# Performance work log

Measured on AMD Instinct MI355X. Metric: run time of the kernel, lower is better.

Reference implementation:

```python
import jax, jax.numpy as jnp
import numpy as np

H = 1024   # hidden_dim
D = 256    # dynamics_dim
L = 2      # gru layers
BS = 1024  # batch
T = 256    # max_len
# activation layout over D: softmax[0:32], softmax[32:47], sigmoid[47:48], sigmoid[48:256]
CAT1 = 32
CAT2_SM_END = 47

def setup_inputs():
    key = jax.random.key(0)
    ks = jax.random.split(key, 12)
    s = 0.02
    return {
        "embed": jax.random.normal(ks[0], (BS, H * (1 + L)), jnp.float32),
        "dynamics": jax.random.uniform(ks[1], (BS, T, D), jnp.float32),
        "seq_len": T,
        "W_ih0": s * jax.random.normal(ks[2], (3 * H, H + D), jnp.float32),
        "W_hh0": s * jax.random.normal(ks[3], (3 * H, H), jnp.float32),
        "b_ih0": s * jax.random.normal(ks[4], (3 * H,), jnp.float32),
        "b_hh0": s * jax.random.normal(ks[5], (3 * H,), jnp.float32),
        "W_ih1": s * jax.random.normal(ks[6], (3 * H, H), jnp.float32),
        "W_hh1": s * jax.random.normal(ks[7], (3 * H, H), jnp.float32),
        "b_ih1": s * jax.random.normal(ks[8], (3 * H,), jnp.float32),
        "b_hh1": s * jax.random.normal(ks[9], (3 * H,), jnp.float32),
        "W_fc": s * jax.random.normal(ks[10], (D, H), jnp.float32),
        "b_fc": s * jax.random.normal(ks[11], (D,), jnp.float32),
    }

def gru_cell(inp, h, W_ih, W_hh, b_ih, b_hh):
    # PyTorch GRU cell math
    gi = inp @ W_ih.T + b_ih          # (bs, 3H)
    gh = h @ W_hh.T + b_hh            # (bs, 3H)
    r = jax.nn.sigmoid(gi[:, :H] + gh[:, :H])
    z = jax.nn.sigmoid(gi[:, H:2 * H] + gh[:, H:2 * H])
    n = jnp.tanh(gi[:, 2 * H:] + r * gh[:, 2 * H:])
    return (1.0 - z) * n + z * h

def apply_activation(x):
    # mirrors processors layout: cat(32), cat-missing(15 softmax + 1 sigmoid), cont(208 sigmoid)
    return jnp.concatenate([
        jax.nn.softmax(x[:, :CAT1], axis=-1),
        jax.nn.softmax(x[:, CAT1:CAT2_SM_END], axis=-1),
        jax.nn.sigmoid(x[:, CAT2_SM_END:]),
    ], axis=-1)

def reference(embed, dynamics, seq_len, W_ih0, W_hh0, b_ih0, b_hh0,
              W_ih1, W_hh1, b_ih1, b_hh1, W_fc, b_fc):
    glob = embed[:, :H]                      # (bs, H)
    h0 = embed[:, H:2 * H]                   # layer-0 initial hidden
    h1 = embed[:, 2 * H:3 * H]               # layer-1 initial hidden
    x0 = dynamics[:, 0, :]                   # (bs, D)

    def step(carry, _):
        x, h0, h1 = carry
        inp = jnp.concatenate([glob, jax.lax.stop_gradient(x)], axis=-1)  # x.detach()
        h0n = gru_cell(inp, h0, W_ih0, W_hh0, b_ih0, b_hh0)
        h1n = gru_cell(h0n, h1, W_ih1, W_hh1, b_ih1, b_hh1)
        out = apply_activation(h1n @ W_fc.T + b_fc)  # (bs, D)
        return (out, h0n, h1n), out

    _, res = jax.lax.scan(step, (x0, h0, h1), None, length=T)
    res = jnp.transpose(res, (1, 0, 2))  # (bs, max_len, D)
    return res
```

## Files before the change

kernel.cpp:

```cpp
#include <hip/hip_runtime.h>
#include <hip/hip_bf16.h>

#define HH    1024
#define DD    256
#define BSB   1024
#define TT    256
#define N3H   3072
#define CAT1  32
#define CAT2E 47

typedef unsigned short u16;
typedef short bf16x8 __attribute__((ext_vector_type(8)));
typedef float f32x4  __attribute__((ext_vector_type(4)));

__device__ __forceinline__ u16 f2bf(float f) {
  unsigned int x = __float_as_uint(f);
  unsigned int lsb = (x >> 16) & 1u;
  x += 0x7fffu + lsb;
  return (u16)(x >> 16);
}

struct GArg {
  const u16* A; int lda; int K;
  const u16* B; int ldb;
  float* C;
  const float* bias;
  const float* addend;
};

#define BM 128
#define BN 128
#define BK 32
#define LDSS 40

__global__ __launch_bounds__(256, 2) void gemm_bt2(GArg ga, GArg gb, int N)
{
  GArg g = (blockIdx.z == 0) ? ga : gb;
  __shared__ __align__(16) u16 As[BM * LDSS];
  __shared__ __align__(16) u16 Bs[BN * LDSS];

  const int tid  = threadIdx.x;
  const int wave = tid >> 6;
  const int lane = tid & 63;
  const int q    = lane >> 4;
  const int l16  = lane & 15;
  const int waveRow = (wave >> 1) * 64;
  const int waveCol = (wave & 1) * 64;
  const int rowBase = blockIdx.y * BM;
  const int colBase = blockIdx.x * BN;

  f32x4 acc[4][4];
  #pragma unroll
  for (int i = 0; i < 4; ++i)
    #pragma unroll
    for (int j = 0; j < 4; ++j)
      acc[i][j] = (f32x4){0.f, 0.f, 0.f, 0.f};

  for (int k0 = 0; k0 < g.K; k0 += BK) {
    __syncthreads();
    #pragma unroll
    for (int it = 0; it < 2; ++it) {
      int li = it * 2048 + tid * 8;
      int r = li >> 5, c = li & 31;
      *(float4*)&As[r * LDSS + c] =
          *(const float4*)(g.A + (size_t)(rowBase + r) * g.lda + k0 + c);
      *(float4*)&Bs[r * LDSS + c] =
          *(const float4*)(g.B + (size_t)(colBase + r) * g.ldb + k0 + c);
    }
    __syncthreads();

    bf16x8 af[4], bfr[4];
    #pragma unroll
    for (int mi = 0; mi < 4; ++mi)
      af[mi] = *(const bf16x8*)&As[(waveRow + mi * 16 + l16) * LDSS + q * 8];
    #pragma unroll
    for (int ni = 0; ni < 4; ++ni)
      bfr[ni] = *(const bf16x8*)&Bs[(waveCol + ni * 16 + l16) * LDSS + q * 8];
    #pragma unroll
    for (int mi = 0; mi < 4; ++mi)
      #pragma unroll
      for (int ni = 0; ni < 4; ++ni)
        acc[mi][ni] = __builtin_amdgcn_mfma_f32_16x16x32_bf16(af[mi], bfr[ni], acc[mi][ni], 0, 0, 0);
  }

  #pragma unroll
  for (int mi = 0; mi < 4; ++mi) {
    #pragma unroll
    for (int ni = 0; ni < 4; ++ni) {
      #pragma unroll
      for (int r = 0; r < 4; ++r) {
        int row = rowBase + waveRow + mi * 16 + q * 4 + r;
        int col = colBase + waveCol + ni * 16 + l16;
        float v = acc[mi][ni][r];
        if (g.bias)   v += g.bias[col];
        if (g.addend) v += g.addend[(size_t)row * N + col];
        g.C[(size_t)row * N + col] = v;
      }
    }
  }
}

__global__ void gate_kernel(const float* __restrict__ GI, const float* __restrict__ GH,
                            float* __restrict__ h, u16* __restrict__ hbf)
{
  int idx = blockIdx.x * blockDim.x + threadIdx.x;
  int b = idx >> 10, m = idx & 1023;
  size_t base = (size_t)b * N3H;
  float gir = GI[base + m], giz = GI[base + HH + m], gin = GI[base + 2 * HH + m];
  float ghr = GH[base + m], ghz = GH[base + HH + m], ghn = GH[base + 2 * HH + m];
  float r = 1.f / (1.f + expf(-(gir + ghr)));
  float z = 1.f / (1.f + expf(-(giz + ghz)));
  float n = tanhf(gin + r * ghn);
  float hv = h[idx];
  float hn = (1.f - z) * n + z * hv;
  h[idx]   = hn;
  hbf[idx] = f2bf(hn);
}

__global__ void act_kernel(const float* __restrict__ logits,
                           float* __restrict__ out, u16* __restrict__ xbf, int t)
{
  int b = blockIdx.x;
  int d = threadIdx.x;
  __shared__ float sv[DD];
  float v = logits[(size_t)b * DD + d];
  sv[d] = v;
  __syncthreads();
  float res;
  if (d < CAT1) {
    float m = -1e30f;
    for (int j = 0; j < CAT1; ++j) m = fmaxf(m, sv[j]);
    float s = 0.f;
    for (int j = 0; j < CAT1; ++j) s += expf(sv[j] - m);
    res = expf(v - m) / s;
  } else if (d < CAT2E) {
    float m = -1e30f;
    for (int j = CAT1; j < CAT2E; ++j) m = fmaxf(m, sv[j]);
    float s = 0.f;
    for (int j = CAT1; j < CAT2E; ++j) s += expf(sv[j] - m);
    res = expf(v - m) / s;
  } else {
    res = 1.f / (1.f + expf(-v));
  }
  out[((size_t)b * TT + t) * DD + d] = res;
  xbf[b * DD + d] = f2bf(res);
}

__global__ void convert_kernel(const float* __restrict__ src, u16* __restrict__ dst, int n)
{
  int i = blockIdx.x * blockDim.x + threadIdx.x;
  if (i < n) dst[i] = f2bf(src[i]);
}

__global__ void prep_state(const float* __restrict__ embed, const float* __restrict__ dyn,
                           u16* __restrict__ globbf,
                           float* __restrict__ h0, u16* __restrict__ h0bf,
                           float* __restrict__ h1, u16* __restrict__ h1bf,
                           u16* __restrict__ xbf)
{
  int idx = blockIdx.x * blockDim.x + threadIdx.x;
  int b = idx >> 10, j = idx & 1023;
  const float* e = embed + (size_t)b * 3072;
  globbf[idx] = f2bf(e[j]);
  float v0 = e[1024 + j]; h0[idx] = v0; h0bf[idx] = f2bf(v0);
  float v1 = e[2048 + j]; h1[idx] = v1; h1bf[idx] = f2bf(v1);
  if (j < DD) {
    xbf[b * DD + j] = f2bf(dyn[(size_t)b * (TT * DD) + j]);
  }
}

extern "C" void kernel_launch(void* const* d_in, const int* in_sizes, int n_in,
                              void* d_out, int out_size, void* d_ws, size_t ws_size,
                              hipStream_t stream)
{
  const float* embed = (const float*)d_in[0];
  const float* dyn   = (const float*)d_in[1];
  const float* W_ih0 = (const float*)d_in[3];
  const float* W_hh0 = (const float*)d_in[4];
  const float* b_ih0 = (const float*)d_in[5];
  const float* b_hh0 = (const float*)d_in[6];
  const float* W_ih1 = (const float*)d_in[7];
  const float* W_hh1 = (const float*)d_in[8];
  const float* b_ih1 = (const float*)d_in[9];
  const float* b_hh1 = (const float*)d_in[10];
  const float* W_fc  = (const float*)d_in[11];
  const float* b_fc  = (const float*)d_in[12];
  float* out = (float*)d_out;

  char* ws = (char*)d_ws;
  size_t off = 0;
  auto carve = [&](size_t bytes) -> void* {
    void* p = ws + off;
    off += (bytes + 255) & ~(size_t)255;
    return p;
  };
  u16* Wih0b = (u16*)carve((size_t)N3H * 1280 * 2);
  u16* Whh0b = (u16*)carve((size_t)N3H * HH * 2);
  u16* Wih1b = (u16*)carve((size_t)N3H * HH * 2);
  u16* Whh1b = (u16*)carve((size_t)N3H * HH * 2);
  u16* Wfcb  = (u16*)carve((size_t)DD * HH * 2);
  u16* globb = (u16*)carve((size_t)BSB * HH * 2);
  u16* xbf   = (u16*)carve((size_t)BSB * DD * 2);
  float* h0f = (float*)carve((size_t)BSB * HH * 4);
  float* h1f = (float*)carve((size_t)BSB * HH * 4);
  u16* h0b   = (u16*)carve((size_t)BSB * HH * 2);
  u16* h1b   = (u16*)carve((size_t)BSB * HH * 2);
  float* Gglob  = (float*)carve((size_t)BSB * N3H * 4);
  float* GI     = (float*)carve((size_t)BSB * N3H * 4);
  float* GHb    = (float*)carve((size_t)BSB * N3H * 4);
  float* logits = (float*)carve((size_t)BSB * DD * 4);
  (void)ws_size;

  {
    int n;
    n = N3H * 1280; convert_kernel<<<(n + 255) / 256, 256, 0, stream>>>(W_ih0, Wih0b, n);
    n = N3H * HH;   convert_kernel<<<(n + 255) / 256, 256, 0, stream>>>(W_hh0, Whh0b, n);
    n = N3H * HH;   convert_kernel<<<(n + 255) / 256, 256, 0, stream>>>(W_ih1, Wih1b, n);
    n = N3H * HH;   convert_kernel<<<(n + 255) / 256, 256, 0, stream>>>(W_hh1, Whh1b, n);
    n = DD * HH;    convert_kernel<<<(n + 255) / 256, 256, 0, stream>>>(W_fc, Wfcb, n);
  }
  prep_state<<<(BSB * HH) / 256, 256, 0, stream>>>(embed, dyn, globb, h0f, h0b, h1f, h1b, xbf);

  {
    GArg g{globb, HH, HH, Wih0b, 1280, Gglob, b_ih0, nullptr};
    gemm_bt2<<<dim3(N3H / BN, BSB / BM, 1), 256, 0, stream>>>(g, g, N3H);
  }

  for (int t = 0; t < TT; ++t) {
    {
      GArg gi{xbf, DD, DD, Wih0b + HH, 1280, GI, nullptr, Gglob};
      GArg gh{h0b, HH, HH, Whh0b, HH, GHb, b_hh0, nullptr};
      gemm_bt2<<<dim3(N3H / BN, BSB / BM, 2), 256, 0, stream>>>(gi, gh, N3H);
    }
    gate_kernel<<<(BSB * HH) / 256, 256, 0, stream>>>(GI, GHb, h0f, h0b);

    {
      GArg gi{h0b, HH, HH, Wih1b, HH, GI, b_ih1, nullptr};
      GArg gh{h1b, HH, HH, Whh1b, HH, GHb, b_hh1, nullptr};
      gemm_bt2<<<dim3(N3H / BN, BSB / BM, 2), 256, 0, stream>>>(gi, gh, N3H);
    }
    gate_kernel<<<(BSB * HH) / 256, 256, 0, stream>>>(GI, GHb, h1f, h1b);

    {
      GArg g{h1b, HH, HH, Wfcb, HH, logits, b_fc, nullptr};
      gemm_bt2<<<dim3(DD / BN, BSB / BM, 1), 256, 0, stream>>>(g, g, DD);
    }
    act_kernel<<<BSB, DD, 0, stream>>>(logits, out, xbf, t);
  }
}
```

Baseline: 31.17 ms.

## Reschedule GRU step GEMMs, use direct-to-LDS loads with swizzle, vectorize gates

The per-step schedule is reordered so each recurrent h@W_hh product for the next step is computed in the same launch as a GEMM the current step already needs. The layer-1 input GEMM is paired with the layer-0 recurrent GEMM, and the fc GEMM with the layer-1 recurrent GEMM. The x-projection GEMM moves to the end of the step. The GEMM kernel switches to global_load_lds 16-byte loads into an XOR-swizzled LDS layout with BK=64 and launch bounds for 3 blocks per CU. The gate kernel is vectorized to float4. These changes aim to cut wasted grid slots, launch count and LDS bank conflicts. The cost is a second GH buffer, and fc blocks beyond N simply return early.

```diff
diff --git a/kernel.cpp b/kernel.cpp
--- a/kernel.cpp
+++ b/kernel.cpp
@@ -1,5 +1,4 @@
 #include <hip/hip_runtime.h>
-#include <hip/hip_bf16.h>
 
 #define HH    1024
 #define DD    256
@@ -20,24 +19,33 @@
   return (u16)(x >> 16);
 }
 
+__device__ __forceinline__ void gload_lds16(const u16* src, u16* lds) {
+  __builtin_amdgcn_global_load_lds(
+      (const __attribute__((address_space(1))) void*)src,
+      (__attribute__((address_space(3))) void*)lds, 16, 0, 0);
+}
+
 struct GArg {
   const u16* A; int lda; int K;
-  const u16* B; int ldb;
-  float* C;
+  const u16* B; int ldb; int N;
+  float* C; int ldc;
   const float* bias;
   const float* addend;
 };
 
 #define BM 128
 #define BN 128
-#define BK 32
-#define LDSS 40
-
-__global__ __launch_bounds__(256, 2) void gemm_bt2(GArg ga, GArg gb, int N)
+#define BK 64
+
+__global__ __launch_bounds__(256, 3) void gemm_bt3(GArg ga, GArg gb)
 {
   GArg g = (blockIdx.z == 0) ? ga : gb;
-  __shared__ __align__(16) u16 As[BM * LDSS];
-  __shared__ __align__(16) u16 Bs[BN * LDSS];
+  const int colBase = blockIdx.x * BN;
+  if (colBase >= g.N) return;
+  const int rowBase = blockIdx.y * BM;
+
+  __shared__ __align__(16) u16 As[BM * BK];
+  __shared__ __align__(16) u16 Bs[BN * BK];
 
   const int tid  = threadIdx.x;
   const int wave = tid >> 6;
@@ -46,8 +54,15 @@
   const int l16  = lane & 15;
   const int waveRow = (wave >> 1) * 64;
   const int waveCol = (wave & 1) * 64;
-  const int rowBase = blockIdx.y * BM;
-  const int colBase = blockIdx.x * BN;
+
+  const int  srow = wave * 8 + (lane >> 3);
+  const int  sswz = ((lane & 7) ^ (lane >> 3)) << 3;
+  const u16* aptr = g.A + (size_t)(rowBase + srow) * g.lda + sswz;
+  const u16* bptr = g.B + (size_t)(colBase + srow) * g.ldb + sswz;
+  const size_t astep = (size_t)32 * g.lda;
+  const size_t bstep = (size_t)32 * g.ldb;
+  u16* aldst = &As[wave << 9];
+  u16* bldst = &Bs[wave << 9];
 
   f32x4 acc[4][4];
   #pragma unroll
@@ -59,28 +74,32 @@
   for (int k0 = 0; k0 < g.K; k0 += BK) {
     __syncthreads();
     #pragma unroll
-    for (int it = 0; it < 2; ++it) {
-      int li = it * 2048 + tid * 8;
-      int r = li >> 5, c = li & 31;
-      *(float4*)&As[r * LDSS + c] =
-          *(const float4*)(g.A + (size_t)(rowBase + r) * g.lda + k0 + c);
-      *(float4*)&Bs[r * LDSS + c] =
-          *(const float4*)(g.B + (size_t)(colBase + r) * g.ldb + k0 + c);
+    for (int i = 0; i < 4; ++i) {
+      gload_lds16(aptr + k0 + (size_t)i * astep, aldst + (i << 11));
+      gload_lds16(bptr + k0 + (size_t)i * bstep, bldst + (i << 11));
     }
     __syncthreads();
 
-    bf16x8 af[4], bfr[4];
     #pragma unroll
-    for (int mi = 0; mi < 4; ++mi)
-      af[mi] = *(const bf16x8*)&As[(waveRow + mi * 16 + l16) * LDSS + q * 8];
-    #pragma unroll
-    for (int ni = 0; ni < 4; ++ni)
-      bfr[ni] = *(const bf16x8*)&Bs[(waveCol + ni * 16 + l16) * LDSS + q * 8];
-    #pragma unroll
-    for (int mi = 0; mi < 4; ++mi)
+    for (int ks = 0; ks < 2; ++ks) {
+      bf16x8 af[4], bfr[4];
+      const int kb = (ks << 2) + q;
       #pragma unroll
-      for (int ni = 0; ni < 4; ++ni)
-        acc[mi][ni] = __builtin_amdgcn_mfma_f32_16x16x32_bf16(af[mi], bfr[ni], acc[mi][ni], 0, 0, 0);
+      for (int mi = 0; mi < 4; ++mi) {
+        int r = waveRow + mi * 16 + l16;
+        af[mi] = *(const bf16x8*)&As[(r << 6) + ((kb ^ (l16 & 7)) << 3)];
+      }
+      #pragma unroll
+      for (int ni = 0; ni < 4; ++ni) {
+        int r = waveCol + ni * 16 + l16;
+        bfr[ni] = *(const bf16x8*)&Bs[(r << 6) + ((kb ^ (l16 & 7)) << 3)];
+      }
+      #pragma unroll
+      for (int mi = 0; mi < 4; ++mi)
+        #pragma unroll
+        for (int ni = 0; ni < 4; ++ni)
+          acc[mi][ni] = __builtin_amdgcn_mfma_f32_16x16x32_bf16(af[mi], bfr[ni], acc[mi][ni], 0, 0, 0);
+    }
   }
 
   #pragma unroll
@@ -93,28 +112,39 @@
         int col = colBase + waveCol + ni * 16 + l16;
         float v = acc[mi][ni][r];
         if (g.bias)   v += g.bias[col];
-        if (g.addend) v += g.addend[(size_t)row * N + col];
-        g.C[(size_t)row * N + col] = v;
+        if (g.addend) v += g.addend[(size_t)row * g.ldc + col];
+        g.C[(size_t)row * g.ldc + col] = v;
       }
     }
   }
 }
 
-__global__ void gate_kernel(const float* __restrict__ GI, const float* __restrict__ GH,
-                            float* __restrict__ h, u16* __restrict__ hbf)
-{
-  int idx = blockIdx.x * blockDim.x + threadIdx.x;
-  int b = idx >> 10, m = idx & 1023;
-  size_t base = (size_t)b * N3H;
-  float gir = GI[base + m], giz = GI[base + HH + m], gin = GI[base + 2 * HH + m];
-  float ghr = GH[base + m], ghz = GH[base + HH + m], ghn = GH[base + 2 * HH + m];
+__device__ __forceinline__ float gate1f(float gir, float ghr, float giz, float ghz,
+                                        float gin, float ghn, float hv) {
   float r = 1.f / (1.f + expf(-(gir + ghr)));
   float z = 1.f / (1.f + expf(-(giz + ghz)));
   float n = tanhf(gin + r * ghn);
-  float hv = h[idx];
-  float hn = (1.f - z) * n + z * hv;
-  h[idx]   = hn;
-  hbf[idx] = f2bf(hn);
+  return (1.f - z) * n + z * hv;
+}
+
+__global__ void gate_kernel(const float4* __restrict__ GI, const float4* __restrict__ GH,
+                            float4* __restrict__ h, ushort4* __restrict__ hbf)
+{
+  int idx = blockIdx.x * blockDim.x + threadIdx.x;
+  int b = idx >> 8, m = idx & 255;
+  size_t base = (size_t)b * 768;
+  float4 gir = GI[base + m], giz = GI[base + 256 + m], gin = GI[base + 512 + m];
+  float4 ghr = GH[base + m], ghz = GH[base + 256 + m], ghn = GH[base + 512 + m];
+  float4 hv = h[idx];
+  float4 hn;
+  hn.x = gate1f(gir.x, ghr.x, giz.x, ghz.x, gin.x, ghn.x, hv.x);
+  hn.y = gate1f(gir.y, ghr.y, giz.y, ghz.y, gin.y, ghn.y, hv.y);
+  hn.z = gate1f(gir.z, ghr.z, giz.z, ghz.z, gin.z, ghn.z, hv.z);
+  hn.w = gate1f(gir.w, ghr.w, giz.w, ghz.w, gin.w, ghn.w, hv.w);
+  h[idx] = hn;
+  ushort4 hb;
+  hb.x = f2bf(hn.x); hb.y = f2bf(hn.y); hb.z = f2bf(hn.z); hb.w = f2bf(hn.w);
+  hbf[idx] = hb;
 }
 
 __global__ void act_kernel(const float* __restrict__ logits,
@@ -207,7 +237,8 @@
   u16* h1b   = (u16*)carve((size_t)BSB * HH * 2);
   float* Gglob  = (float*)carve((size_t)BSB * N3H * 4);
   float* GI     = (float*)carve((size_t)BSB * N3H * 4);
-  float* GHb    = (float*)carve((size_t)BSB * N3H * 4);
+  float* GH0f   = (float*)carve((size_t)BSB * N3H * 4);
+  float* GH1f   = (float*)carve((size_t)BSB * N3H * 4);
   float* logits = (float*)carve((size_t)BSB * DD * 4);
   (void)ws_size;
 
@@ -221,30 +252,49 @@
   }
   prep_state<<<(BSB * HH) / 256, 256, 0, stream>>>(embed, dyn, globb, h0f, h0b, h1f, h1b, xbf);
 
+  const dim3 G1(N3H / BN, BSB / BM, 1);
+  const dim3 G2(N3H / BN, BSB / BM, 2);
+
   {
-    GArg g{globb, HH, HH, Wih0b, 1280, Gglob, b_ih0, nullptr};
-    gemm_bt2<<<dim3(N3H / BN, BSB / BM, 1), 256, 0, stream>>>(g, g, N3H);
+    GArg g{globb, HH, HH, Wih0b, 1280, N3H, Gglob, N3H, b_ih0, nullptr};
+    gemm_bt3<<<G1, 256, 0, stream>>>(g, g);
+  }
+  {
+    GArg ga{h0b, HH, HH, Whh0b, HH, N3H, GH0f, N3H, b_hh0, nullptr};
+    GArg gb{h1b, HH, HH, Whh1b, HH, N3H, GH1f, N3H, b_hh1, nullptr};
+    gemm_bt3<<<G2, 256, 0, stream>>>(ga, gb);
+  }
+  {
+    GArg g{xbf, DD, DD, Wih0b + HH, 1280, N3H, GI, N3H, nullptr, Gglob};
+    gemm_bt3<<<G1, 256, 0, stream>>>(g, g);
   }
 
   for (int t = 0; t < TT; ++t) {
+    bool last = (t == TT - 1);
+
+    gate_kernel<<<(BSB * HH / 4) / 256, 256, 0, stream>>>(
+        (const float4*)GI, (const float4*)GH0f, (float4*)h0f, (ushort4*)h0b);
+
     {
-      GArg gi{xbf, DD, DD, Wih0b + HH, 1280, GI, nullptr, Gglob};
-      GArg gh{h0b, HH, HH, Whh0b, HH, GHb, b_hh0, nullptr};
-      gemm_bt2<<<dim3(N3H / BN, BSB / BM, 2), 256, 0, stream>>>(gi, gh, N3H);
-    }
-    gate_kernel<<<(BSB * HH) / 256, 256, 0, stream>>>(GI, GHb, h0f, h0b);
+      GArg gi{h0b, HH, HH, Wih1b, HH, N3H, GI, N3H, b_ih1, nullptr};
+      GArg gh{h0b, HH, HH, Whh0b, HH, N3H, GH0f, N3H, b_hh0, nullptr};
+      gemm_bt3<<<last ? G1 : G2, 256, 0, stream>>>(gi, gh);
+    }
+
+    gate_kernel<<<(BSB * HH / 4) / 256, 256, 0, stream>>>(
+        (const float4*)GI, (const float4*)GH1f, (float4*)h1f, (ushort4*)h1b);
 
     {
-      GArg gi{h0b, HH, HH, Wih1b, HH, GI, b_ih1, nullptr};
-      GArg gh{h1b, HH, HH, Whh1b, HH, GHb, b_hh1, nullptr};
-      gemm_bt2<<<dim3(N3H / BN, BSB / BM, 2), 256, 0, stream>>>(gi, gh, N3H);
-    }
-    gate_kernel<<<(BSB * HH) / 256, 256, 0, stream>>>(GI, GHb, h1f, h1b);
-
-    {
-      GArg g{h1b, HH, HH, Wfcb, HH, logits, b_fc, nullptr};
-      gemm_bt2<<<dim3(DD / BN, BSB / BM, 1), 256, 0, stream>>>(g, g, DD);
-    }
+      GArg gc{h1b, HH, HH, Wfcb, HH, DD, logits, DD, b_fc, nullptr};
+      GArg gh{h1b, HH, HH, Whh1b, HH, N3H, GH1f, N3H, b_hh1, nullptr};
+      gemm_bt3<<<last ? G1 : G2, 256, 0, stream>>>(gc, gh);
+    }
+
     act_kernel<<<BSB, DD, 0, stream>>>(logits, out, xbf, t);
-  }
-}
+
+    if (!last) {
+      GArg g{xbf, DD, DD, Wih0b + HH, 1280, N3H, GI, N3H, nullptr, Gglob};
+      gemm_bt3<<<G1, 256, 0, stream>>>(g, g);
+    }
+  }
+}
```

New measurement: 25.18 ms. -19.2%, faster.
